# Kernel tuning notes

Measured on AMD Instinct MI355X. Metric: run time of the kernel, lower is better.

## Reference

```python
import jax, jax.numpy as jnp
import numpy as np

BATCH, SEQ = 2, 4096
IN_FEATURES = 4096
OUT_FEATURES = 4096
BLOCK = 64                      # oft_block_size (bs)
RANK = IN_FEATURES // BLOCK     # number of diagonal blocks (r)


def setup_inputs() -> dict:
    key = jax.random.key(0)
    k1, k2, k3, k4 = jax.random.split(key, 4)
    x = jax.random.normal(k1, (BATCH, SEQ, IN_FEATURES), dtype=jnp.float32)
    # OFT adapter parameters: one (bs x bs) generator per block
    oft_r = jax.random.normal(k2, (RANK, BLOCK, BLOCK), dtype=jnp.float32) * 0.02
    # Dequantized GPTQ weight (out_features x in_features) + bias
    W = jax.random.normal(k3, (OUT_FEATURES, IN_FEATURES), dtype=jnp.float32) * 0.02
    b = jax.random.normal(k4, (OUT_FEATURES,), dtype=jnp.float32)
    return {"x": x, "oft_r": oft_r, "W": W, "b": b}


def _cayley_batch(data):
    # data: [r, bs, bs].  Q = (I - skew) @ (I + skew)^{-1}  (torch.linalg.solve left=False)
    bs = data.shape[-1]
    skew = 0.5 * (data - jnp.swapaxes(data, -1, -2))
    I = jnp.eye(bs, dtype=data.dtype)
    A = I + skew   # [r, bs, bs]
    B = I - skew
    # Solve Q A = B  ->  A^T Q^T = B^T
    Qt = jnp.linalg.solve(jnp.swapaxes(A, -1, -2), jnp.swapaxes(B, -1, -2))
    return jnp.swapaxes(Qt, -1, -2)


def reference(x, oft_r, W, b):
    rank, bs, _ = oft_r.shape
    # oft_rotation starts as identity; single active adapter -> rotation = Cayley(oft_r)
    oft_rotation = _cayley_batch(oft_r)            # [rank, bs, bs]
    batch_dims = x.shape[:-1]
    x_reshaped = x.reshape(*batch_dims, rank, bs)  # [..., r, k]
    x_rot = jnp.einsum('...rk,rkc->...rc', x_reshaped, oft_rotation)
    x_rot = x_rot.reshape(*batch_dims, rank * bs)  # [..., in_features]
    # quant_linear_module (dequantized): y = x_rot @ W^T + b
    return jnp.einsum('bsi,oi->bso', x_rot, W) + b
```

## Files before the change

kernel.cpp:

```cpp
#include <hip/hip_runtime.h>
#include <hip/hip_bf16.h>
#include <stdint.h>


typedef __bf16 bf16;
typedef __attribute__((ext_vector_type(4))) __bf16 bf16x4;
typedef __attribute__((ext_vector_type(8))) __bf16 bf16x8;
typedef __attribute__((ext_vector_type(4))) float f32x4;

__device__ __forceinline__ bf16 f2bf(float f) {
  unsigned u = __builtin_bit_cast(unsigned, f);
  u += 0x7fffu + ((u >> 16) & 1u);
  unsigned short h = (unsigned short)(u >> 16);
  return __builtin_bit_cast(bf16, h);
}

__global__ __launch_bounds__(256) void cayley_kernel(const float* __restrict__ oft_r,
                                                     float* __restrict__ Qxt) {
  __shared__ float S[64][65];
  __shared__ float Ta[64][65];
  __shared__ float Tb[64][65];
  const int tid = threadIdx.x;
  const int r = blockIdx.x;
  const float* D = oft_r + (size_t)r * 4096;

  for (int idx = tid; idx < 4096; idx += 256) {
    int i = idx >> 6, j = idx & 63;
    float s = 0.5f * (D[i * 64 + j] - D[j * 64 + i]);
    S[i][j] = s;
    Ta[i][j] = (i == j ? 1.0f : 0.0f) - s;
  }
  __syncthreads();

  const int j = tid & 63;
  const int w = tid >> 6;
  float (*Tin)[65] = Ta;
  float (*Tout)[65] = Tb;

  for (int it = 0; it < 5; ++it) {
    float tcol[64];
#pragma unroll
    for (int c = 0; c < 64; ++c) tcol[c] = Tin[c][j];
    float out[16];
    for (int m = 0; m < 16; ++m) {
      int i = w * 16 + m;
      float s = 0.f;
#pragma unroll
      for (int c = 0; c < 64; ++c) s += S[i][c] * tcol[c];
      out[m] = (i == j ? 1.0f : 0.0f) - s;
    }
    for (int m = 0; m < 16; ++m) Tout[w * 16 + m][j] = out[m];
    __syncthreads();
    float (*tmp)[65] = Tin; Tin = Tout; Tout = tmp;
  }
  {
    float tcol[64];
#pragma unroll
    for (int c = 0; c < 64; ++c) tcol[c] = Tin[c][j];
    for (int m = 0; m < 16; ++m) {
      int i = w * 16 + m;
      float s = 0.f;
#pragma unroll
      for (int c = 0; c < 64; ++c) s += S[i][c] * tcol[c];
      Qxt[(size_t)r * 4096 + i * 64 + j] = Tin[i][j] - s;
    }
  }
}

__global__ __launch_bounds__(256) void fold_w_kernel(const float* __restrict__ W,
                                                     const float* __restrict__ Qxt,
                                                     bf16* __restrict__ Wp) {
  __shared__ bf16 Wb[128 * 64];
  __shared__ bf16 Xt[64 * 64];
  const int tid = threadIdx.x;
  const int lane = tid & 63;
  const int wave = tid >> 6;
  const int o0 = blockIdx.x * 128;
  const int r = blockIdx.y;
  const int fr = lane & 15;
  const int kg = lane >> 4;

#pragma unroll
  for (int i = 0; i < 8; ++i) {
    int c = i * 256 + tid;
    int row = c >> 4, c4 = c & 15;
    f32x4 v = *reinterpret_cast<const f32x4*>(W + (size_t)(o0 + row) * 4096 + r * 64 + c4 * 4);
    bf16x4 o; o[0] = f2bf(v[0]); o[1] = f2bf(v[1]); o[2] = f2bf(v[2]); o[3] = f2bf(v[3]);
    *reinterpret_cast<bf16x4*>(&Wb[row * 64 + c4 * 4]) = o;
  }
#pragma unroll
  for (int i = 0; i < 4; ++i) {
    int c = i * 256 + tid;
    int row = c >> 4, c4 = c & 15;
    f32x4 v = *reinterpret_cast<const f32x4*>(Qxt + (size_t)r * 4096 + row * 64 + c4 * 4);
    bf16x4 o; o[0] = f2bf(v[0]); o[1] = f2bf(v[1]); o[2] = f2bf(v[2]); o[3] = f2bf(v[3]);
    *reinterpret_cast<bf16x4*>(&Xt[row * 64 + c4 * 4]) = o;
  }
  __syncthreads();

  const int wm = wave * 32;
  f32x4 acc[2][4];
#pragma unroll
  for (int mi = 0; mi < 2; ++mi)
#pragma unroll
    for (int ni = 0; ni < 4; ++ni) acc[mi][ni] = (f32x4){0.f, 0.f, 0.f, 0.f};

#pragma unroll
  for (int kk = 0; kk < 64; kk += 32) {
    bf16x8 af[2], bx[4];
#pragma unroll
    for (int mi = 0; mi < 2; ++mi)
      af[mi] = *reinterpret_cast<const bf16x8*>(&Wb[(wm + mi * 16 + fr) * 64 + kk + kg * 8]);
#pragma unroll
    for (int ni = 0; ni < 4; ++ni)
      bx[ni] = *reinterpret_cast<const bf16x8*>(&Xt[(ni * 16 + fr) * 64 + kk + kg * 8]);
#pragma unroll
    for (int mi = 0; mi < 2; ++mi)
#pragma unroll
      for (int ni = 0; ni < 4; ++ni)
        acc[mi][ni] = __builtin_amdgcn_mfma_f32_16x16x32_bf16(af[mi], bx[ni], acc[mi][ni], 0, 0, 0);
  }

#pragma unroll
  for (int mi = 0; mi < 2; ++mi)
#pragma unroll
    for (int ni = 0; ni < 4; ++ni)
#pragma unroll
      for (int q = 0; q < 4; ++q) {
        int row = o0 + wm + mi * 16 + kg * 4 + q;
        int col = ni * 16 + fr;
        Wp[(size_t)row * 4096 + r * 64 + col] = f2bf(acc[mi][ni][q]);
      }
}

__global__ __launch_bounds__(256) void cast_x_kernel(const float* __restrict__ x,
                                                     bf16* __restrict__ xb, long n) {
  long i0 = ((long)blockIdx.x * 256 + threadIdx.x) * 8;
  long stride = (long)gridDim.x * 256 * 8;
  for (long i = i0; i < n; i += stride) {
    f32x4 a = *reinterpret_cast<const f32x4*>(x + i);
    f32x4 b = *reinterpret_cast<const f32x4*>(x + i + 4);
    bf16x8 o;
    o[0] = f2bf(a[0]); o[1] = f2bf(a[1]); o[2] = f2bf(a[2]); o[3] = f2bf(a[3]);
    o[4] = f2bf(b[0]); o[5] = f2bf(b[1]); o[6] = f2bf(b[2]); o[7] = f2bf(b[3]);
    *reinterpret_cast<bf16x8*>(xb + i) = o;
  }
}


#define GLDS16(g, l) __builtin_amdgcn_global_load_lds( \
    (const __attribute__((address_space(1))) unsigned int*)(g), \
    (__attribute__((address_space(3))) unsigned int*)(l), 16, 0, 0)

#define VMCNT4 asm volatile("s_waitcnt vmcnt(4)" ::: "memory")
#define VMCNT0 asm volatile("s_waitcnt vmcnt(0)" ::: "memory")
#define BARRIER() do { asm volatile("" ::: "memory"); \
  __builtin_amdgcn_s_barrier(); asm volatile("" ::: "memory"); } while (0)

__global__ __launch_bounds__(512, 2) void gemm_kernel(const bf16* __restrict__ A,
                                                      const bf16* __restrict__ B,
                                                      const float* __restrict__ bias,
                                                      float* __restrict__ C,
                                                      int M, int N, int K) {
  __shared__ bf16 lds[65536];
  const int tid = threadIdx.x;
  const int lane = tid & 63;
  const int wave = tid >> 6;
  const int wr = wave >> 2;
  const int wc = wave & 3;
  const int fr = lane & 15;
  const int kg = lane >> 4;
  const int m0 = blockIdx.y * 256;
  const int n0 = blockIdx.x * 256;
  const int NT = K >> 6;

  f32x4 acc[8][4];
#pragma unroll
  for (int m = 0; m < 8; ++m)
#pragma unroll
    for (int n = 0; n < 4; ++n) acc[m][n] = (f32x4){0.f, 0.f, 0.f, 0.f};

  auto STAGE = [&](int t, int p) {
    const int op = p & 1, ks = p >> 1;
    const bf16* src = op ? B : A;
    const int base_row = op ? n0 : m0;
    const int ldsb = (t & 1) * 32768 + op * 16384 + ks * 8192;
#pragma unroll
    for (int i = 0; i < 2; ++i) {
      int c = i * 512 + tid;
      int row = c >> 2, cc = c & 3;
      const bf16* g = src + (size_t)(base_row + row) * K + t * 64 + ks * 32
                      + ((cc ^ ((row >> 1) & 3)) << 3);
      GLDS16(g, &lds[ldsb + ((i * 512 + wave * 64) << 3)]);
    }
  };
  auto LDA = [&](int buf, int ks, int mi) -> bf16x8 {
    int row = wr * 128 + mi * 16 + fr;
    return *reinterpret_cast<const bf16x8*>(
        &lds[buf * 32768 + ks * 8192 + row * 32 + ((kg ^ ((row >> 1) & 3)) << 3)]);
  };
  auto LDB = [&](int buf, int ks, int ni) -> bf16x8 {
    int row = wc * 64 + ni * 16 + fr;
    return *reinterpret_cast<const bf16x8*>(
        &lds[buf * 32768 + 16384 + ks * 8192 + row * 32 + ((kg ^ ((row >> 1) & 3)) << 3)]);
  };

#pragma unroll
  for (int p = 0; p < 4; ++p) STAGE(0, p);
  VMCNT4;
  BARRIER();

  bf16x8 afr[4], bfr[4];
  for (int t = 0; t < NT; ++t) {
    const int bc = t & 1;
    const bool pre = (t + 1 < NT);

    if (pre) STAGE(t + 1, 0);
#pragma unroll
    for (int n = 0; n < 4; ++n) bfr[n] = LDB(bc, 0, n);
#pragma unroll
    for (int m = 0; m < 4; ++m) afr[m] = LDA(bc, 0, m);
    BARRIER();
    __builtin_amdgcn_s_setprio(1);
#pragma unroll
    for (int m = 0; m < 4; ++m)
#pragma unroll
      for (int n = 0; n < 4; ++n)
        acc[m][n] = __builtin_amdgcn_mfma_f32_16x16x32_bf16(afr[m], bfr[n], acc[m][n], 0, 0, 0);
    __builtin_amdgcn_s_setprio(0);

    if (pre) STAGE(t + 1, 1);
#pragma unroll
    for (int m = 0; m < 4; ++m) afr[m] = LDA(bc, 0, 4 + m);
    if (pre) { VMCNT4; } else { VMCNT0; }
    BARRIER();
    __builtin_amdgcn_s_setprio(1);
#pragma unroll
    for (int m = 0; m < 4; ++m)
#pragma unroll
      for (int n = 0; n < 4; ++n)
        acc[4 + m][n] = __builtin_amdgcn_mfma_f32_16x16x32_bf16(afr[m], bfr[n], acc[4 + m][n], 0, 0, 0);
    __builtin_amdgcn_s_setprio(0);

    if (pre) STAGE(t + 1, 2);
#pragma unroll
    for (int n = 0; n < 4; ++n) bfr[n] = LDB(bc, 1, n);
#pragma unroll
    for (int m = 0; m < 4; ++m) afr[m] = LDA(bc, 1, m);
    BARRIER();
    __builtin_amdgcn_s_setprio(1);
#pragma unroll
    for (int m = 0; m < 4; ++m)
#pragma unroll
      for (int n = 0; n < 4; ++n)
        acc[m][n] = __builtin_amdgcn_mfma_f32_16x16x32_bf16(afr[m], bfr[n], acc[m][n], 0, 0, 0);
    __builtin_amdgcn_s_setprio(0);

    if (pre) STAGE(t + 1, 3);
#pragma unroll
    for (int m = 0; m < 4; ++m) afr[m] = LDA(bc, 1, 4 + m);
    if (pre) { VMCNT4; } else { VMCNT0; }
    BARRIER();
    __builtin_amdgcn_s_setprio(1);
#pragma unroll
    for (int m = 0; m < 4; ++m)
#pragma unroll
      for (int n = 0; n < 4; ++n)
        acc[4 + m][n] = __builtin_amdgcn_mfma_f32_16x16x32_bf16(afr[m], bfr[n], acc[4 + m][n], 0, 0, 0);
    __builtin_amdgcn_s_setprio(0);
  }

#pragma unroll
  for (int n = 0; n < 4; ++n) {
    int col = n0 + wc * 64 + n * 16 + fr;
    float bv = bias[col];
#pragma unroll
    for (int m = 0; m < 8; ++m) {
      int row0 = m0 + wr * 128 + m * 16 + kg * 4;
#pragma unroll
      for (int q = 0; q < 4; ++q)
        C[(size_t)(row0 + q) * N + col] = acc[m][n][q] + bv;
    }
  }
}

extern "C" void kernel_launch(void* const* d_in, const int* in_sizes, int n_in,
                              void* d_out, int out_size, void* d_ws, size_t ws_size,
                              hipStream_t stream) {
  const float* x     = (const float*)d_in[0];
  const float* oft_r = (const float*)d_in[1];
  const float* W     = (const float*)d_in[2];
  const float* b     = (const float*)d_in[3];
  float* y = (float*)d_out;

  char* ws = (char*)d_ws;
  float* Qxt = (float*)ws;
  bf16*  Wp  = (bf16*)(ws + (1u << 20));
  bf16*  xb  = (bf16*)(ws + (1u << 20) + (32u << 20));

  cayley_kernel<<<64, 256, 0, stream>>>(oft_r, Qxt);
  dim3 fg(32, 64);
  fold_w_kernel<<<fg, 256, 0, stream>>>(W, Qxt, Wp);
  cast_x_kernel<<<2048, 256, 0, stream>>>(x, xb, 33554432L);
  dim3 gg(4096 / 256, 8192 / 256);
  gemm_kernel<<<gg, 512, 0, stream>>>(xb, Wp, b, y, 8192, 4096, 4096);
}
```

Before: 364.0 us.

## Restructure GEMM main loop into unrolled double-buffer tiles; vectorize Cayley iteration

The GEMM K-loop is unrolled by two with macro tiles that use static buffer indices and separate fragment registers, moves global-to-LDS staging after the fragment reads, and adds a barrier after each MFMA block. The Cayley kernel now stores the skew matrix transposed and computes as an outer product, reading S with vector LDS loads instead of keeping a 64-entry column in registers. The GEMM change aims to give the compiler a cleaner schedule and better overlap of loads with MFMA, at the cost of extra barriers and higher register pressure. The Cayley change cuts register use and LDS load count in a small prologue kernel.

```diff
diff --git a/kernel.cpp b/kernel.cpp
--- a/kernel.cpp
+++ b/kernel.cpp
@@ -17,7 +17,7 @@
 
 __global__ __launch_bounds__(256) void cayley_kernel(const float* __restrict__ oft_r,
                                                      float* __restrict__ Qxt) {
-  __shared__ float S[64][65];
+  __shared__ float St[64][68];
   __shared__ float Ta[64][65];
   __shared__ float Tb[64][65];
   const int tid = threadIdx.x;
@@ -27,7 +27,7 @@
   for (int idx = tid; idx < 4096; idx += 256) {
     int i = idx >> 6, j = idx & 63;
     float s = 0.5f * (D[i * 64 + j] - D[j * 64 + i]);
-    S[i][j] = s;
+    St[j][i] = s;
     Ta[i][j] = (i == j ? 1.0f : 0.0f) - s;
   }
   __syncthreads();
@@ -38,32 +38,48 @@
   float (*Tout)[65] = Tb;
 
   for (int it = 0; it < 5; ++it) {
-    float tcol[64];
-#pragma unroll
-    for (int c = 0; c < 64; ++c) tcol[c] = Tin[c][j];
     float out[16];
-    for (int m = 0; m < 16; ++m) {
-      int i = w * 16 + m;
-      float s = 0.f;
-#pragma unroll
-      for (int c = 0; c < 64; ++c) s += S[i][c] * tcol[c];
-      out[m] = (i == j ? 1.0f : 0.0f) - s;
+#pragma unroll
+    for (int m = 0; m < 16; ++m) out[m] = ((w * 16 + m) == j ? 1.0f : 0.0f);
+    for (int c = 0; c < 64; ++c) {
+      float tc = Tin[c][j];
+      f32x4 s0 = *reinterpret_cast<const f32x4*>(&St[c][w * 16]);
+      f32x4 s1 = *reinterpret_cast<const f32x4*>(&St[c][w * 16 + 4]);
+      f32x4 s2 = *reinterpret_cast<const f32x4*>(&St[c][w * 16 + 8]);
+      f32x4 s3 = *reinterpret_cast<const f32x4*>(&St[c][w * 16 + 12]);
+#pragma unroll
+      for (int q = 0; q < 4; ++q) {
+        out[q]      -= s0[q] * tc;
+        out[4 + q]  -= s1[q] * tc;
+        out[8 + q]  -= s2[q] * tc;
+        out[12 + q] -= s3[q] * tc;
+      }
     }
+#pragma unroll
     for (int m = 0; m < 16; ++m) Tout[w * 16 + m][j] = out[m];
     __syncthreads();
     float (*tmp)[65] = Tin; Tin = Tout; Tout = tmp;
   }
   {
-    float tcol[64];
-#pragma unroll
-    for (int c = 0; c < 64; ++c) tcol[c] = Tin[c][j];
-    for (int m = 0; m < 16; ++m) {
-      int i = w * 16 + m;
-      float s = 0.f;
-#pragma unroll
-      for (int c = 0; c < 64; ++c) s += S[i][c] * tcol[c];
-      Qxt[(size_t)r * 4096 + i * 64 + j] = Tin[i][j] - s;
+    float out[16];
+#pragma unroll
+    for (int m = 0; m < 16; ++m) out[m] = Tin[w * 16 + m][j];
+    for (int c = 0; c < 64; ++c) {
+      float tc = Tin[c][j];
+      f32x4 s0 = *reinterpret_cast<const f32x4*>(&St[c][w * 16]);
+      f32x4 s1 = *reinterpret_cast<const f32x4*>(&St[c][w * 16 + 4]);
+      f32x4 s2 = *reinterpret_cast<const f32x4*>(&St[c][w * 16 + 8]);
+      f32x4 s3 = *reinterpret_cast<const f32x4*>(&St[c][w * 16 + 12]);
+#pragma unroll
+      for (int q = 0; q < 4; ++q) {
+        out[q]      -= s0[q] * tc;
+        out[4 + q]  -= s1[q] * tc;
+        out[8 + q]  -= s2[q] * tc;
+        out[12 + q] -= s3[q] * tc;
+      }
     }
+#pragma unroll
+    for (int m = 0; m < 16; ++m) Qxt[(size_t)r * 4096 + (w * 16 + m) * 64 + j] = out[m];
   }
 }
 
@@ -156,6 +172,44 @@
 #define VMCNT0 asm volatile("s_waitcnt vmcnt(0)" ::: "memory")
 #define BARRIER() do { asm volatile("" ::: "memory"); \
   __builtin_amdgcn_s_barrier(); asm volatile("" ::: "memory"); } while (0)
+
+#define MFMA16(AF, BF, RB) \
+  _Pragma("unroll") \
+  for (int m_ = 0; m_ < 4; ++m_) \
+    _Pragma("unroll") \
+    for (int n_ = 0; n_ < 4; ++n_) \
+      acc[RB + m_][n_] = __builtin_amdgcn_mfma_f32_16x16x32_bf16(AF[m_], BF[n_], acc[RB + m_][n_], 0, 0, 0);
+
+#define DO_TILE(BUF, TN, PRE) do { \
+     \
+    _Pragma("unroll") for (int n_ = 0; n_ < 4; ++n_) Ob[n_] = LDB(BUF, 0, n_); \
+    _Pragma("unroll") for (int m_ = 0; m_ < 4; ++m_) Oa[m_] = LDA(BUF, 0, m_); \
+    if (PRE) STAGE(TN, BUF ^ 1, 0); \
+    BARRIER(); \
+    __builtin_amdgcn_s_setprio(1); MFMA16(Oa, Ob, 0) __builtin_amdgcn_s_setprio(0); \
+    BARRIER(); \
+     \
+    _Pragma("unroll") for (int m_ = 0; m_ < 4; ++m_) Ea[m_] = LDA(BUF, 0, 4 + m_); \
+    if (PRE) STAGE(TN, BUF ^ 1, 1); \
+    if (PRE) { VMCNT4; } else { VMCNT0; } \
+    BARRIER(); \
+    __builtin_amdgcn_s_setprio(1); MFMA16(Ea, Ob, 4) __builtin_amdgcn_s_setprio(0); \
+    BARRIER(); \
+     \
+    _Pragma("unroll") for (int n_ = 0; n_ < 4; ++n_) Eb[n_] = LDB(BUF, 1, n_); \
+    _Pragma("unroll") for (int m_ = 0; m_ < 4; ++m_) Oa[m_] = LDA(BUF, 1, m_); \
+    if (PRE) STAGE(TN, BUF ^ 1, 2); \
+    BARRIER(); \
+    __builtin_amdgcn_s_setprio(1); MFMA16(Oa, Eb, 0) __builtin_amdgcn_s_setprio(0); \
+    BARRIER(); \
+     \
+    _Pragma("unroll") for (int m_ = 0; m_ < 4; ++m_) Ea[m_] = LDA(BUF, 1, 4 + m_); \
+    if (PRE) STAGE(TN, BUF ^ 1, 3); \
+    if (PRE) { VMCNT4; } else { VMCNT0; } \
+    BARRIER(); \
+    __builtin_amdgcn_s_setprio(1); MFMA16(Ea, Eb, 4) __builtin_amdgcn_s_setprio(0); \
+    BARRIER(); \
+  } while (0)
 
 __global__ __launch_bounds__(512, 2) void gemm_kernel(const bf16* __restrict__ A,
                                                       const bf16* __restrict__ B,
@@ -180,11 +234,11 @@
 #pragma unroll
     for (int n = 0; n < 4; ++n) acc[m][n] = (f32x4){0.f, 0.f, 0.f, 0.f};
 
-  auto STAGE = [&](int t, int p) {
+  auto STAGE = [&](int t, int db, int p) {
     const int op = p & 1, ks = p >> 1;
     const bf16* src = op ? B : A;
     const int base_row = op ? n0 : m0;
-    const int ldsb = (t & 1) * 32768 + op * 16384 + ks * 8192;
+    const int ldsb = db * 32768 + op * 16384 + ks * 8192;
 #pragma unroll
     for (int i = 0; i < 2; ++i) {
       int c = i * 512 + tid;
@@ -206,68 +260,14 @@
   };
 
 #pragma unroll
-  for (int p = 0; p < 4; ++p) STAGE(0, p);
+  for (int p = 0; p < 4; ++p) STAGE(0, 0, p);
   VMCNT4;
   BARRIER();
 
-  bf16x8 afr[4], bfr[4];
-  for (int t = 0; t < NT; ++t) {
-    const int bc = t & 1;
-    const bool pre = (t + 1 < NT);
-
-    if (pre) STAGE(t + 1, 0);
-#pragma unroll
-    for (int n = 0; n < 4; ++n) bfr[n] = LDB(bc, 0, n);
-#pragma unroll
-    for (int m = 0; m < 4; ++m) afr[m] = LDA(bc, 0, m);
-    BARRIER();
-    __builtin_amdgcn_s_setprio(1);
-#pragma unroll
-    for (int m = 0; m < 4; ++m)
-#pragma unroll
-      for (int n = 0; n < 4; ++n)
-        acc[m][n] = __builtin_amdgcn_mfma_f32_16x16x32_bf16(afr[m], bfr[n], acc[m][n], 0, 0, 0);
-    __builtin_amdgcn_s_setprio(0);
-
-    if (pre) STAGE(t + 1, 1);
-#pragma unroll
-    for (int m = 0; m < 4; ++m) afr[m] = LDA(bc, 0, 4 + m);
-    if (pre) { VMCNT4; } else { VMCNT0; }
-    BARRIER();
-    __builtin_amdgcn_s_setprio(1);
-#pragma unroll
-    for (int m = 0; m < 4; ++m)
-#pragma unroll
-      for (int n = 0; n < 4; ++n)
-        acc[4 + m][n] = __builtin_amdgcn_mfma_f32_16x16x32_bf16(afr[m], bfr[n], acc[4 + m][n], 0, 0, 0);
-    __builtin_amdgcn_s_setprio(0);
-
-    if (pre) STAGE(t + 1, 2);
-#pragma unroll
-    for (int n = 0; n < 4; ++n) bfr[n] = LDB(bc, 1, n);
-#pragma unroll
-    for (int m = 0; m < 4; ++m) afr[m] = LDA(bc, 1, m);
-    BARRIER();
-    __builtin_amdgcn_s_setprio(1);
-#pragma unroll
-    for (int m = 0; m < 4; ++m)
-#pragma unroll
-      for (int n = 0; n < 4; ++n)
-        acc[m][n] = __builtin_amdgcn_mfma_f32_16x16x32_bf16(afr[m], bfr[n], acc[m][n], 0, 0, 0);
-    __builtin_amdgcn_s_setprio(0);
-
-    if (pre) STAGE(t + 1, 3);
-#pragma unroll
-    for (int m = 0; m < 4; ++m) afr[m] = LDA(bc, 1, 4 + m);
-    if (pre) { VMCNT4; } else { VMCNT0; }
-    BARRIER();
-    __builtin_amdgcn_s_setprio(1);
-#pragma unroll
-    for (int m = 0; m < 4; ++m)
-#pragma unroll
-      for (int n = 0; n < 4; ++n)
-        acc[4 + m][n] = __builtin_amdgcn_mfma_f32_16x16x32_bf16(afr[m], bfr[n], acc[4 + m][n], 0, 0, 0);
-    __builtin_amdgcn_s_setprio(0);
+  bf16x8 Oa[4], Ob[4], Ea[4], Eb[4];
+  for (int t = 0; t < NT; t += 2) {
+    DO_TILE(0, t + 1, true);
+    DO_TILE(1, t + 2, (t + 2) < NT);
   }
 
 #pragma unroll
```

After: 341.3 us. 1.07x faster.
